# Kernel optimization log

Hardware: AMD Instinct MI355X
Metric: run time of the kernel (lower is better)

The kernel has to match this reference:

```python
import jax, jax.numpy as jnp
import numpy as np

N = 50000      # nodes
E = 400000     # edges
D_IN = 128     # input node feature dim
H = 128        # hidden_dim == node_dim inside layers
E_DIM = 16     # edge_attr dim
L = 3          # num_layers


def setup_inputs() -> dict:
    key = jax.random.key(0)
    ks = jax.random.split(key, 8)
    s = 0.05
    return {
        "x": jax.random.normal(ks[0], (N, D_IN), jnp.float32),
        "edge_attr": jax.random.normal(ks[1], (E, E_DIM), jnp.float32),
        "edge_index": jax.random.randint(ks[2], (2, E), 0, N),
        # learned params (W stored [in, out], i.e. transpose of torch Linear.weight)
        "proj_W": jax.random.normal(ks[3], (D_IN, H), jnp.float32) * s,
        "proj_b": jnp.zeros((H,), jnp.float32),
        "msg_W1": jax.random.normal(ks[4], (L, 2 * H + E_DIM, H), jnp.float32) * s,
        "msg_b1": jnp.zeros((L, H), jnp.float32),
        "msg_W2": jax.random.normal(ks[5], (L, H, H), jnp.float32) * s,
        "msg_b2": jnp.zeros((L, H), jnp.float32),
        "upd_W": jax.random.normal(ks[6], (L, 2 * H, H), jnp.float32) * s,
        "upd_b": jnp.zeros((L, H), jnp.float32),
        "ln_g": jnp.ones((L, H), jnp.float32),
        "ln_b": jnp.zeros((L, H), jnp.float32),
        "out_g": jnp.ones((H,), jnp.float32),
        "out_b": jnp.zeros((H,), jnp.float32),
    }


def _layernorm(x, g, b, eps=1e-5):
    mu = jnp.mean(x, axis=-1, keepdims=True)
    var = jnp.mean((x - mu) ** 2, axis=-1, keepdims=True)
    return (x - mu) * jax.lax.rsqrt(var + eps) * g + b


def reference(x, edge_attr, edge_index, proj_W, proj_b, msg_W1, msg_b1,
              msg_W2, msg_b2, upd_W, upd_b, ln_g, ln_b, out_g, out_b):
    i_idx, j_idx = edge_index[0], edge_index[1]
    h = x @ proj_W + proj_b                       # [N, H]
    for l in range(L):                            # fixed small layer count
        # gather + message MLP: m_ij = relu(relu([h_i, h_j, e_ij] W1) W2)
        m_in = jnp.concatenate([h[i_idx], h[j_idx], edge_attr], axis=-1)  # [E, 2H+E_DIM]
        m = jax.nn.relu(m_in @ msg_W1[l] + msg_b1[l])
        m = jax.nn.relu(m @ msg_W2[l] + msg_b2[l])  # [E, H]
        # scatter-add aggregate to destination nodes (index_add_ on i_idx)
        agg = jax.ops.segment_sum(m, i_idx, num_segments=N)  # [N, H]
        # node update MLP + residual + LayerNorm (dropout p inactive in eval)
        out = jax.nn.relu(jnp.concatenate([h, agg], axis=-1) @ upd_W[l] + upd_b[l])
        h = _layernorm(out + h, ln_g[l], ln_b[l])
    h = _layernorm(h, out_g, out_b)
    return jnp.mean(h, axis=0)[None, :]           # global mean pool -> [1, H]
```

## Files before the change

kernel.cpp:

```cpp
#include <hip/hip_runtime.h>
#include <math.h>

#define N_NODES 50000
#define N_EDGES 400000
#define DIM_IN  128
#define H       128
#define E_DIM   16
#define NLAYERS 3

#define K1      272
#define K1P     288
#define HS      136
#define GS      136
#define ES      40
#define US      264
#define PS      136
#define FPS     132
#define MB      32
#define UMB     64
#define NT_E    (N_EDGES / MB)
#define NSB     ((N_NODES + 255) / 256)

typedef short  s16x8 __attribute__((ext_vector_type(8)));
typedef float  f32x4 __attribute__((ext_vector_type(4)));

__device__ inline unsigned short f2bf(float f) {
    union { float f; unsigned u; } v; v.f = f;
    unsigned r = v.u + 0x7FFFu + ((v.u >> 16) & 1u);
    return (unsigned short)(r >> 16);
}
__device__ inline float bf2f(unsigned short u) {
    union { unsigned u; float f; } v; v.u = (unsigned)u << 16; return v.f;
}
__device__ inline uint4 addbf8(uint4 a, uint4 b) {
    union U { uint4 v; unsigned short s[8]; } ua, ub, uo;
    ua.v = a; ub.v = b;
#pragma unroll
    for (int i = 0; i < 8; ++i) uo.s[i] = f2bf(bf2f(ua.s[i]) + bf2f(ub.s[i]));
    return uo.v;
}

__global__ __launch_bounds__(256)
void convert_w1(const float* __restrict__ W1, unsigned short* __restrict__ W1t)
{
    const int o = blockIdx.x * 256 + threadIdx.x;
    const int l = o / (128 * K1P);
    const int r = o % (128 * K1P);
    const int n = r / K1P;
    const int k = r % K1P;
    const float v = (k < K1) ? W1[(size_t)l * K1 * H + (size_t)k * H + n] : 0.f;
    W1t[o] = f2bf(v);
}

__global__ __launch_bounds__(256)
void convert_w2(const float* __restrict__ W2, unsigned short* __restrict__ W2t)
{
    const int o = blockIdx.x * 256 + threadIdx.x;
    const int l = o / (H * H);
    const int r = o % (H * H);
    const int n = r / H;
    const int k = r % H;
    W2t[o] = f2bf(W2[(size_t)l * H * H + (size_t)k * H + n]);
}

__global__ __launch_bounds__(256)
void convert_wu(const float* __restrict__ Wu, unsigned short* __restrict__ Wut)
{
    const int o = blockIdx.x * 256 + threadIdx.x;
    const int l = o / (H * 256);
    const int r = o % (H * 256);
    const int n = r / 256;
    const int k = r % 256;
    Wut[o] = f2bf(Wu[(size_t)l * 256 * H + (size_t)k * H + n]);
}

__global__ __launch_bounds__(256)
void convert_wp(const float* __restrict__ Wp, unsigned short* __restrict__ Wpt)
{
    const int o = blockIdx.x * 256 + threadIdx.x;
    const int n = o / H;
    const int k = o % H;
    Wpt[o] = f2bf(Wp[(size_t)k * H + n]);
}

__global__ __launch_bounds__(256)
void convert_ea(const float* __restrict__ ea, const int* __restrict__ perm,
                unsigned short* __restrict__ eabf)
{
    const int o = blockIdx.x * 256 + threadIdx.x;
    const int p = o >> 3;
    const int j = (o & 7) * 2;
    const int pe = perm[p];
    const float2 v = *(const float2*)&ea[(size_t)pe * E_DIM + j];
    eabf[(size_t)p * E_DIM + j]     = f2bf(v.x);
    eabf[(size_t)p * E_DIM + j + 1] = f2bf(v.y);
}

__global__ __launch_bounds__(256)
void hist_kernel(const int* __restrict__ ei, int* __restrict__ hist)
{
    const int e = blockIdx.x * 256 + threadIdx.x;
    if (e < N_EDGES) atomicAdd(&hist[ei[e]], 1);
}

__global__ __launch_bounds__(256)
void blocksum_kernel(const int* __restrict__ hist, int* __restrict__ bsum)
{
    __shared__ int red[4];
    const int t = threadIdx.x;
    const int idx = blockIdx.x * 256 + t;
    int v = (idx < N_NODES) ? hist[idx] : 0;
#pragma unroll
    for (int off = 32; off > 0; off >>= 1) v += __shfl_xor(v, off, 64);
    if ((t & 63) == 0) red[t >> 6] = v;
    __syncthreads();
    if (t == 0) bsum[blockIdx.x] = red[0] + red[1] + red[2] + red[3];
}

__global__ __launch_bounds__(256)
void scan_bsum_kernel(const int* __restrict__ bsum, int* __restrict__ boff)
{
    __shared__ int s[256];
    const int t = threadIdx.x;
    const int v = (t < NSB) ? bsum[t] : 0;
    s[t] = v; __syncthreads();
    for (int off = 1; off < 256; off <<= 1) {
        const int u = (t >= off) ? s[t - off] : 0;
        __syncthreads();
        s[t] += u;
        __syncthreads();
    }
    if (t < NSB) boff[t] = s[t] - v;
}

__global__ __launch_bounds__(256)
void scan_final_kernel(const int* __restrict__ hist, const int* __restrict__ boff,
                       int* __restrict__ cursor)
{
    __shared__ int s[256];
    const int t = threadIdx.x;
    const int idx = blockIdx.x * 256 + t;
    const int v = (idx < N_NODES) ? hist[idx] : 0;
    s[t] = v; __syncthreads();
    for (int off = 1; off < 256; off <<= 1) {
        const int u = (t >= off) ? s[t - off] : 0;
        __syncthreads();
        s[t] += u;
        __syncthreads();
    }
    if (idx < N_NODES) cursor[idx] = boff[blockIdx.x] + s[t] - v;
}

__global__ __launch_bounds__(256)
void scatter_kernel(const int* __restrict__ ei, int* __restrict__ cursor,
                    int* __restrict__ i_s, int* __restrict__ j_s, int* __restrict__ perm)
{
    const int e = blockIdx.x * 256 + threadIdx.x;
    if (e < N_EDGES) {
        const int d = ei[e];
        const int p = atomicAdd(&cursor[d], 1);
        i_s[p] = d;
        j_s[p] = ei[N_EDGES + e];
        perm[p] = e;
    }
}

__global__ __launch_bounds__(256)
void proj_mfma(const float* __restrict__ x, const unsigned short* __restrict__ Wpt,
               const float* __restrict__ b, unsigned short* __restrict__ hbf)
{
    __shared__ __align__(16) unsigned short A[MB][PS];
    const int tid = threadIdx.x;
    const int n0 = blockIdx.x * MB;
    const int wave = tid >> 6, lane = tid & 63, l15 = lane & 15, l4 = lane >> 4;
    const int colbase = wave * 32;

#pragma unroll
    for (int i = 0; i < 4; ++i) {
        const int f = tid + i * 256;
        const int row = f >> 5, c4 = f & 31;
        const int node = min(n0 + row, N_NODES - 1);
        const float4 v = *((const float4*)(x + (size_t)node * DIM_IN) + c4);
        unsigned short o[4] = { f2bf(v.x), f2bf(v.y), f2bf(v.z), f2bf(v.w) };
        *(uint2*)&A[row][c4 * 4] = *(const uint2*)o;
    }
    __syncthreads();

    f32x4 acc[2][2];
#pragma unroll
    for (int mt = 0; mt < 2; ++mt)
#pragma unroll
        for (int nt = 0; nt < 2; ++nt) acc[mt][nt] = (f32x4)0.f;

    for (int k = 0; k < DIM_IN; k += 32) {
        const s16x8 a0 = *(const s16x8*)&A[l15][k + l4 * 8];
        const s16x8 a1 = *(const s16x8*)&A[16 + l15][k + l4 * 8];
        const s16x8 b0 = *(const s16x8*)&Wpt[(size_t)(colbase + l15) * DIM_IN + k + l4 * 8];
        const s16x8 b1 = *(const s16x8*)&Wpt[(size_t)(colbase + 16 + l15) * DIM_IN + k + l4 * 8];
        acc[0][0] = __builtin_amdgcn_mfma_f32_16x16x32_bf16(a0, b0, acc[0][0], 0, 0, 0);
        acc[0][1] = __builtin_amdgcn_mfma_f32_16x16x32_bf16(a0, b1, acc[0][1], 0, 0, 0);
        acc[1][0] = __builtin_amdgcn_mfma_f32_16x16x32_bf16(a1, b0, acc[1][0], 0, 0, 0);
        acc[1][1] = __builtin_amdgcn_mfma_f32_16x16x32_bf16(a1, b1, acc[1][1], 0, 0, 0);
    }

    const float bi0 = b[colbase + l15], bi1 = b[colbase + 16 + l15];
#pragma unroll
    for (int mt = 0; mt < 2; ++mt)
#pragma unroll
        for (int r = 0; r < 4; ++r) {
            const int row = mt * 16 + l4 * 4 + r;
            const int n = n0 + row;
            if (n < N_NODES) {
                hbf[(size_t)n * H + colbase + l15]      = f2bf(acc[mt][0][r] + bi0);
                hbf[(size_t)n * H + colbase + 16 + l15] = f2bf(acc[mt][1][r] + bi1);
            }
        }
}

__global__ __launch_bounds__(256)
void premul(const unsigned short* __restrict__ hbf,
            const unsigned short* __restrict__ W1t,
            unsigned short* __restrict__ Pa, unsigned short* __restrict__ Pb)
{
    __shared__ __align__(16) unsigned short A[MB][PS];
    const int tid = threadIdx.x;
    const int n0 = blockIdx.x * MB;
    const int wave = tid >> 6, lane = tid & 63, l15 = lane & 15, l4 = lane >> 4;
    const int colbase = wave * 32;

#pragma unroll
    for (int i = 0; i < 2; ++i) {
        const int f = tid + i * 256;
        const int row = f >> 4, c = f & 15;
        const int node = min(n0 + row, N_NODES - 1);
        const uint4 v = *((const uint4*)(hbf + (size_t)node * H) + c);
        *(uint4*)&A[row][c * 8] = v;
    }
    __syncthreads();

    f32x4 aa[2][2], ab[2][2];
#pragma unroll
    for (int mt = 0; mt < 2; ++mt)
#pragma unroll
        for (int nt = 0; nt < 2; ++nt) { aa[mt][nt] = (f32x4)0.f; ab[mt][nt] = (f32x4)0.f; }

#pragma unroll
    for (int kt = 0; kt < 4; ++kt) {
        const s16x8 a0 = *(const s16x8*)&A[l15][kt * 32 + l4 * 8];
        const s16x8 a1 = *(const s16x8*)&A[16 + l15][kt * 32 + l4 * 8];
        const s16x8 wa0 = *(const s16x8*)&W1t[(size_t)(colbase + l15) * K1P + kt * 32 + l4 * 8];
        const s16x8 wa1 = *(const s16x8*)&W1t[(size_t)(colbase + 16 + l15) * K1P + kt * 32 + l4 * 8];
        const s16x8 wb0 = *(const s16x8*)&W1t[(size_t)(colbase + l15) * K1P + 128 + kt * 32 + l4 * 8];
        const s16x8 wb1 = *(const s16x8*)&W1t[(size_t)(colbase + 16 + l15) * K1P + 128 + kt * 32 + l4 * 8];
        aa[0][0] = __builtin_amdgcn_mfma_f32_16x16x32_bf16(a0, wa0, aa[0][0], 0, 0, 0);
        aa[0][1] = __builtin_amdgcn_mfma_f32_16x16x32_bf16(a0, wa1, aa[0][1], 0, 0, 0);
        aa[1][0] = __builtin_amdgcn_mfma_f32_16x16x32_bf16(a1, wa0, aa[1][0], 0, 0, 0);
        aa[1][1] = __builtin_amdgcn_mfma_f32_16x16x32_bf16(a1, wa1, aa[1][1], 0, 0, 0);
        ab[0][0] = __builtin_amdgcn_mfma_f32_16x16x32_bf16(a0, wb0, ab[0][0], 0, 0, 0);
        ab[0][1] = __builtin_amdgcn_mfma_f32_16x16x32_bf16(a0, wb1, ab[0][1], 0, 0, 0);
        ab[1][0] = __builtin_amdgcn_mfma_f32_16x16x32_bf16(a1, wb0, ab[1][0], 0, 0, 0);
        ab[1][1] = __builtin_amdgcn_mfma_f32_16x16x32_bf16(a1, wb1, ab[1][1], 0, 0, 0);
    }

#pragma unroll
    for (int mt = 0; mt < 2; ++mt)
#pragma unroll
        for (int r = 0; r < 4; ++r) {
            const int row = mt * 16 + l4 * 4 + r;
            const int n = n0 + row;
            if (n < N_NODES) {
                Pa[(size_t)n * H + colbase + l15]      = f2bf(aa[mt][0][r]);
                Pa[(size_t)n * H + colbase + 16 + l15] = f2bf(aa[mt][1][r]);
                Pb[(size_t)n * H + colbase + l15]      = f2bf(ab[mt][0][r]);
                Pb[(size_t)n * H + colbase + 16 + l15] = f2bf(ab[mt][1][r]);
            }
        }
}

__global__ __launch_bounds__(256, 4)
void edge_kernel(const unsigned short* __restrict__ Pa,
                 const unsigned short* __restrict__ Pb,
                 const unsigned short* __restrict__ eabf,
                 const int*   __restrict__ i_s,
                 const int*   __restrict__ j_s,
                 const unsigned short* __restrict__ W1t,
                 const float* __restrict__ b1,
                 const unsigned short* __restrict__ W2t,
                 const float* __restrict__ b2,
                 float*       __restrict__ agg)
{
    __shared__ __align__(16) unsigned short Gsum[MB * GS];
    __shared__ __align__(16) unsigned short Et[MB * ES];
    __shared__ __align__(16) unsigned short Hid[MB * HS];
    __shared__ __align__(16) unsigned short Mbf[MB * HS];
    __shared__ int idxbuf[2][MB];

    const int tid  = threadIdx.x;
    const int wave = tid >> 6;
    const int lane = tid & 63;
    const int l15  = lane & 15;
    const int l4   = lane >> 4;
    const int colbase = wave * 32;

    const int sl_e = tid >> 4;
    const int sl_c = tid & 15;

    s16x8 w2f[2][4], w1cf[2];
#pragma unroll
    for (int kt = 0; kt < 4; ++kt) {
        w2f[0][kt] = *(const s16x8*)&W2t[(size_t)(colbase + l15) * H + kt * 32 + l4 * 8];
        w2f[1][kt] = *(const s16x8*)&W2t[(size_t)(colbase + 16 + l15) * H + kt * 32 + l4 * 8];
    }
    w1cf[0] = *(const s16x8*)&W1t[(size_t)(colbase + l15) * K1P + 256 + l4 * 8];
    w1cf[1] = *(const s16x8*)&W1t[(size_t)(colbase + 16 + l15) * K1P + 256 + l4 * 8];
    const float b1c0 = b1[colbase + l15], b1c1 = b1[colbase + 16 + l15];
    const float b2c0 = b2[colbase + l15], b2c1 = b2[colbase + 16 + l15];

    int t = blockIdx.x;
    if (t >= NT_E) return;

    {
#pragma unroll
        for (int i = 0; i < 2; ++i) {
            const int e = sl_e + i * 16;
            const int ni = i_s[t * MB + e];
            const int nj = j_s[t * MB + e];
            const uint4 va = *((const uint4*)(Pa + (size_t)ni * H) + sl_c);
            const uint4 vb = *((const uint4*)(Pb + (size_t)nj * H) + sl_c);
            *(uint4*)&Gsum[e * GS + sl_c * 8] = addbf8(va, vb);
        }
        if (tid < 64) {
            const uint4 ve = *((const uint4*)eabf + (size_t)t * 64 + tid);
            *(uint4*)&Et[(tid >> 1) * ES + (tid & 1) * 8] = ve;
        } else if (tid < 128) {
            const int tt = tid - 64;
            const uint4 z = {0, 0, 0, 0};
            *(uint4*)&Et[(tt >> 1) * ES + 16 + (tt & 1) * 8] = z;
        }
        if (tid < MB) idxbuf[0][tid] = i_s[t * MB + tid];
    }
    __syncthreads();

    int p = 0;
    for (; t < NT_E; t += gridDim.x, p ^= 1) {
        const int t1 = t + gridDim.x;

        uint4 pfa[2], pfb[2];
        uint4 pfe = {0, 0, 0, 0};
        int   pfi = 0;
        if (t1 < NT_E) {
#pragma unroll
            for (int i = 0; i < 2; ++i) {
                const int e = sl_e + i * 16;
                const int ni = i_s[t1 * MB + e];
                const int nj = j_s[t1 * MB + e];
                pfa[i] = *((const uint4*)(Pa + (size_t)ni * H) + sl_c);
                pfb[i] = *((const uint4*)(Pb + (size_t)nj * H) + sl_c);
            }
            if (tid < 64) pfe = *((const uint4*)eabf + (size_t)t1 * 64 + tid);
            if (tid < MB) pfi = i_s[t1 * MB + tid];
        }

        f32x4 acc[2][2];
#pragma unroll
        for (int mt = 0; mt < 2; ++mt)
#pragma unroll
            for (int nt = 0; nt < 2; ++nt) acc[mt][nt] = (f32x4)0.f;
        {
            const s16x8 a0 = *(const s16x8*)&Et[l15 * ES + l4 * 8];
            const s16x8 a1 = *(const s16x8*)&Et[(16 + l15) * ES + l4 * 8];
            acc[0][0] = __builtin_amdgcn_mfma_f32_16x16x32_bf16(a0, w1cf[0], acc[0][0], 0, 0, 0);
            acc[0][1] = __builtin_amdgcn_mfma_f32_16x16x32_bf16(a0, w1cf[1], acc[0][1], 0, 0, 0);
            acc[1][0] = __builtin_amdgcn_mfma_f32_16x16x32_bf16(a1, w1cf[0], acc[1][0], 0, 0, 0);
            acc[1][1] = __builtin_amdgcn_mfma_f32_16x16x32_bf16(a1, w1cf[1], acc[1][1], 0, 0, 0);
        }

#pragma unroll
        for (int mt = 0; mt < 2; ++mt)
#pragma unroll
            for (int r = 0; r < 4; ++r) {
                const int row = mt * 16 + l4 * 4 + r;
                const float g0 = bf2f(Gsum[row * GS + colbase + l15]);
                const float g1 = bf2f(Gsum[row * GS + colbase + 16 + l15]);
                Hid[row * HS + colbase + l15]      = f2bf(fmaxf(acc[mt][0][r] + g0 + b1c0, 0.f));
                Hid[row * HS + colbase + 16 + l15] = f2bf(fmaxf(acc[mt][1][r] + g1 + b1c1, 0.f));
            }
        __syncthreads();

        if (t1 < NT_E) {
#pragma unroll
            for (int i = 0; i < 2; ++i) {
                const int e = sl_e + i * 16;
                *(uint4*)&Gsum[e * GS + sl_c * 8] = addbf8(pfa[i], pfb[i]);
            }
            if (tid < 64)
                *(uint4*)&Et[(tid >> 1) * ES + (tid & 1) * 8] = pfe;
            if (tid < MB) idxbuf[p ^ 1][tid] = pfi;
        }

#pragma unroll
        for (int mt = 0; mt < 2; ++mt)
#pragma unroll
            for (int nt = 0; nt < 2; ++nt) acc[mt][nt] = (f32x4)0.f;

#pragma unroll
        for (int kt = 0; kt < 4; ++kt) {
            const s16x8 a0 = *(const s16x8*)&Hid[l15 * HS + kt * 32 + l4 * 8];
            const s16x8 a1 = *(const s16x8*)&Hid[(16 + l15) * HS + kt * 32 + l4 * 8];
            acc[0][0] = __builtin_amdgcn_mfma_f32_16x16x32_bf16(a0, w2f[0][kt], acc[0][0], 0, 0, 0);
            acc[0][1] = __builtin_amdgcn_mfma_f32_16x16x32_bf16(a0, w2f[1][kt], acc[0][1], 0, 0, 0);
            acc[1][0] = __builtin_amdgcn_mfma_f32_16x16x32_bf16(a1, w2f[0][kt], acc[1][0], 0, 0, 0);
            acc[1][1] = __builtin_amdgcn_mfma_f32_16x16x32_bf16(a1, w2f[1][kt], acc[1][1], 0, 0, 0);
        }

#pragma unroll
        for (int mt = 0; mt < 2; ++mt)
#pragma unroll
            for (int r = 0; r < 4; ++r) {
                const int row = mt * 16 + l4 * 4 + r;
                Mbf[row * HS + colbase + l15]      = f2bf(fmaxf(acc[mt][0][r] + b2c0, 0.f));
                Mbf[row * HS + colbase + 16 + l15] = f2bf(fmaxf(acc[mt][1][r] + b2c1, 0.f));
            }
        __syncthreads();

        {
            const int* idxp = idxbuf[p];
            const int c    = tid & 127;
            const int half = tid >> 7;
            int cur = idxp[half * 16];
            float s = 0.f;
            for (int r = half * 16; r < half * 16 + 16; ++r) {
                const int d = idxp[r];
                if (d != cur) {
                    atomicAdd(&agg[(size_t)cur * H + c], s);
                    s = 0.f; cur = d;
                }
                s += bf2f(Mbf[r * HS + c]);
            }
            atomicAdd(&agg[(size_t)cur * H + c], s);
        }
    }
}

__global__ __launch_bounds__(256, 3)
void update_mfma(unsigned short* __restrict__ hbf, float* __restrict__ agg,
                 const unsigned short* __restrict__ Wut, const float* __restrict__ b,
                 const float* __restrict__ g, const float* __restrict__ bln)
{
    __shared__ __align__(16) unsigned short A[UMB][US];
    float* Afp = (float*)&A[0][0];

    const int tid = threadIdx.x;
    const int n0 = blockIdx.x * UMB;
    const int wave = tid >> 6, lane = tid & 63, l15 = lane & 15, l4 = lane >> 4;
    const int colbase = wave * 32;

    s16x8 bf0[8], bf1[8];
#pragma unroll
    for (int kt = 0; kt < 8; ++kt) {
        bf0[kt] = *(const s16x8*)&Wut[(size_t)(colbase + l15) * 256 + kt * 32 + l4 * 8];
        bf1[kt] = *(const s16x8*)&Wut[(size_t)(colbase + 16 + l15) * 256 + kt * 32 + l4 * 8];
    }

#pragma unroll
    for (int i = 0; i < 4; ++i) {
        const int f = tid + i * 256;
        const int row = f >> 4, c = f & 15;
        const int node = min(n0 + row, N_NODES - 1);
        const uint4 v = *((const uint4*)(hbf + (size_t)node * H) + c);
        *(uint4*)&A[row][c * 8] = v;
    }
#pragma unroll
    for (int i = 0; i < 8; ++i) {
        const int f = tid + i * 256;
        const int row = f >> 5, c4 = f & 31;
        const int node = min(n0 + row, N_NODES - 1);
        float4* ap = (float4*)(agg + (size_t)node * H) + c4;
        const float4 v = *ap;
        if (n0 + row < N_NODES) {
            const float4 z = {0.f, 0.f, 0.f, 0.f};
            *ap = z;
        }
        unsigned short o[4] = { f2bf(v.x), f2bf(v.y), f2bf(v.z), f2bf(v.w) };
        *(uint2*)&A[row][128 + c4 * 4] = *(const uint2*)o;
    }
    __syncthreads();

    f32x4 acc[4][2];
#pragma unroll
    for (int mt = 0; mt < 4; ++mt) { acc[mt][0] = (f32x4)0.f; acc[mt][1] = (f32x4)0.f; }

#pragma unroll
    for (int kt = 0; kt < 8; ++kt) {
#pragma unroll
        for (int mt = 0; mt < 4; ++mt) {
            const s16x8 a = *(const s16x8*)&A[mt * 16 + l15][kt * 32 + l4 * 8];
            acc[mt][0] = __builtin_amdgcn_mfma_f32_16x16x32_bf16(a, bf0[kt], acc[mt][0], 0, 0, 0);
            acc[mt][1] = __builtin_amdgcn_mfma_f32_16x16x32_bf16(a, bf1[kt], acc[mt][1], 0, 0, 0);
        }
    }
    __syncthreads();

    {
        const float bi0 = b[colbase + l15], bi1 = b[colbase + 16 + l15];
#pragma unroll
        for (int mt = 0; mt < 4; ++mt)
#pragma unroll
            for (int r = 0; r < 4; ++r) {
                const int row = mt * 16 + l4 * 4 + r;
                Afp[row * FPS + colbase + l15]      = fmaxf(acc[mt][0][r] + bi0, 0.f);
                Afp[row * FPS + colbase + 16 + l15] = fmaxf(acc[mt][1][r] + bi1, 0.f);
            }
    }
    __syncthreads();

    const float g0 = g[lane],   g1 = g[64 + lane];
    const float l0 = bln[lane], l1 = bln[64 + lane];
    for (int q = 0; q < 16; ++q) {
        const int row = wave * 16 + q;
        const int n = n0 + row;
        if (n >= N_NODES) break;
        const float hr0 = bf2f(hbf[(size_t)n * H + lane]);
        const float hr1 = bf2f(hbf[(size_t)n * H + 64 + lane]);
        float v0 = Afp[row * FPS + lane]      + hr0;
        float v1 = Afp[row * FPS + 64 + lane] + hr1;
        float s = v0 + v1;
#pragma unroll
        for (int off = 32; off > 0; off >>= 1) s += __shfl_xor(s, off, 64);
        const float mu = s * (1.f / 128.f);
        const float d0 = v0 - mu, d1 = v1 - mu;
        float vs = d0 * d0 + d1 * d1;
#pragma unroll
        for (int off = 32; off > 0; off >>= 1) vs += __shfl_xor(vs, off, 64);
        const float inv = rsqrtf(vs * (1.f / 128.f) + 1e-5f);
        hbf[(size_t)n * H + lane]      = f2bf(d0 * inv * g0 + l0);
        hbf[(size_t)n * H + 64 + lane] = f2bf(d1 * inv * g1 + l1);
    }
}

__global__ __launch_bounds__(256)
void final_kernel(const unsigned short* __restrict__ hbf,
                  const float* __restrict__ g, const float* __restrict__ b,
                  float* __restrict__ out)
{
    __shared__ float red[4][128];
    const int tid = threadIdx.x;
    const int wave = tid >> 6, lane = tid & 63;
    const float g0 = g[lane], g1 = g[64 + lane];
    const float b0 = b[lane], b1 = b[64 + lane];
    float a0 = 0.f, a1 = 0.f;

    for (int n = blockIdx.x * 4 + wave; n < N_NODES; n += gridDim.x * 4) {
        const float v0 = bf2f(hbf[(size_t)n * H + lane]);
        const float v1 = bf2f(hbf[(size_t)n * H + 64 + lane]);
        float s = v0 + v1;
#pragma unroll
        for (int off = 32; off > 0; off >>= 1) s += __shfl_xor(s, off, 64);
        const float mu = s * (1.f / 128.f);
        const float d0 = v0 - mu, d1 = v1 - mu;
        float vs = d0 * d0 + d1 * d1;
#pragma unroll
        for (int off = 32; off > 0; off >>= 1) vs += __shfl_xor(vs, off, 64);
        const float inv = rsqrtf(vs * (1.f / 128.f) + 1e-5f);
        a0 += d0 * inv * g0 + b0;
        a1 += d1 * inv * g1 + b1;
    }
    red[wave][lane]      = a0;
    red[wave][64 + lane] = a1;
    __syncthreads();
    if (wave == 0) {
        const float s0 = red[0][lane] + red[1][lane] + red[2][lane] + red[3][lane];
        const float s1 = red[0][64 + lane] + red[1][64 + lane] + red[2][64 + lane] + red[3][64 + lane];
        atomicAdd(&out[lane],      s0 * (1.f / N_NODES));
        atomicAdd(&out[64 + lane], s1 * (1.f / N_NODES));
    }
}

extern "C" void kernel_launch(void* const* d_in, const int* in_sizes, int n_in,
                              void* d_out, int out_size, void* d_ws, size_t ws_size,
                              hipStream_t stream)
{
    const float* x         = (const float*)d_in[0];
    const float* edge_attr = (const float*)d_in[1];
    const int*   edge_idx  = (const int*)  d_in[2];
    const float* proj_W    = (const float*)d_in[3];
    const float* proj_b    = (const float*)d_in[4];
    const float* msg_W1    = (const float*)d_in[5];
    const float* msg_b1    = (const float*)d_in[6];
    const float* msg_W2    = (const float*)d_in[7];
    const float* msg_b2    = (const float*)d_in[8];
    const float* upd_W     = (const float*)d_in[9];
    const float* upd_b     = (const float*)d_in[10];
    const float* ln_g      = (const float*)d_in[11];
    const float* ln_b      = (const float*)d_in[12];
    const float* out_g     = (const float*)d_in[13];
    const float* out_b     = (const float*)d_in[14];
    float* out = (float*)d_out;

    char* w = (char*)d_ws;
    float* agg = (float*)w;                   w += (size_t)N_NODES * H * 4;
    unsigned short* hbf  = (unsigned short*)w; w += (size_t)N_NODES * H * 2;
    unsigned short* Pa   = (unsigned short*)w; w += (size_t)N_NODES * H * 2;
    unsigned short* Pb   = (unsigned short*)w; w += (size_t)N_NODES * H * 2;
    unsigned short* eabf = (unsigned short*)w; w += (size_t)N_EDGES * E_DIM * 2;
    unsigned short* W1t  = (unsigned short*)w; w += (size_t)NLAYERS * H * K1P * 2;
    unsigned short* W2t  = (unsigned short*)w; w += (size_t)NLAYERS * H * H * 2;
    unsigned short* Wut  = (unsigned short*)w; w += (size_t)NLAYERS * H * 256 * 2;
    unsigned short* Wpt  = (unsigned short*)w; w += (size_t)H * DIM_IN * 2;
    int* hist   = (int*)w;                    w += (size_t)N_NODES * 4;
    int* cursor = (int*)w;                    w += (size_t)N_NODES * 4;
    int* bsum   = (int*)w;                    w += (size_t)256 * 4;
    int* boff   = (int*)w;                    w += (size_t)256 * 4;
    int* i_s    = (int*)w;                    w += (size_t)N_EDGES * 4;
    int* j_s    = (int*)w;                    w += (size_t)N_EDGES * 4;
    int* perm   = (int*)w;                    w += (size_t)N_EDGES * 4;

    convert_w1<<<(NLAYERS * H * K1P) / 256, 256, 0, stream>>>(msg_W1, W1t);
    convert_w2<<<(NLAYERS * H * H) / 256, 256, 0, stream>>>(msg_W2, W2t);
    convert_wu<<<(NLAYERS * H * 256) / 256, 256, 0, stream>>>(upd_W, Wut);
    convert_wp<<<(H * DIM_IN) / 256, 256, 0, stream>>>(proj_W, Wpt);

    hipMemsetAsync(hist, 0, (size_t)N_NODES * 4, stream);
    hipMemsetAsync(agg, 0, (size_t)N_NODES * H * sizeof(float), stream);
    hist_kernel<<<(N_EDGES + 255) / 256, 256, 0, stream>>>(edge_idx, hist);
    blocksum_kernel<<<NSB, 256, 0, stream>>>(hist, bsum);
    scan_bsum_kernel<<<1, 256, 0, stream>>>(bsum, boff);
    scan_final_kernel<<<NSB, 256, 0, stream>>>(hist, boff, cursor);
    scatter_kernel<<<(N_EDGES + 255) / 256, 256, 0, stream>>>(edge_idx, cursor, i_s, j_s, perm);
    convert_ea<<<(N_EDGES * 8) / 256, 256, 0, stream>>>(edge_attr, perm, eabf);

    const int nblk = (N_NODES + MB - 1) / MB;
    proj_mfma<<<nblk, 256, 0, stream>>>(x, Wpt, proj_b, hbf);

    const int ublk = (N_NODES + UMB - 1) / UMB;
    for (int l = 0; l < NLAYERS; ++l) {
        premul<<<nblk, 256, 0, stream>>>(hbf, W1t + (size_t)l * H * K1P, Pa, Pb);
        edge_kernel<<<1024, 256, 0, stream>>>(
            Pa, Pb, eabf, i_s, j_s,
            W1t + (size_t)l * H * K1P, msg_b1 + (size_t)l * H,
            W2t + (size_t)l * H * H,   msg_b2 + (size_t)l * H, agg);
        update_mfma<<<ublk, 256, 0, stream>>>(
            hbf, agg, Wut + (size_t)l * H * 256, upd_b + (size_t)l * H,
            ln_g + (size_t)l * H, ln_b + (size_t)l * H);
    }

    hipMemsetAsync(out, 0, H * sizeof(float), stream);
    final_kernel<<<256, 256, 0, stream>>>(hbf, out_g, out_b, out);
}
```

Baseline: 535.7 us.

## Switch edge-kernel intermediates to fp16 and scatter directly from MFMA accumulators

```diff
diff --git a/kernel.cpp b/kernel.cpp
--- a/kernel.cpp
+++ b/kernel.cpp
@@ -11,8 +11,8 @@
 #define K1      272
 #define K1P     288
 #define HS      136
-#define GS      136
-#define ES      40
+#define GSH     136
+#define ETS     32
 #define US      264
 #define PS      136
 #define FPS     132
@@ -21,8 +21,10 @@
 #define NT_E    (N_EDGES / MB)
 #define NSB     ((N_NODES + 255) / 256)
 
-typedef short  s16x8 __attribute__((ext_vector_type(8)));
-typedef float  f32x4 __attribute__((ext_vector_type(4)));
+typedef short    s16x8 __attribute__((ext_vector_type(8)));
+typedef float    f32x4 __attribute__((ext_vector_type(4)));
+typedef _Float16 f16x8 __attribute__((ext_vector_type(8)));
+typedef __fp16   fp16x2 __attribute__((ext_vector_type(2)));
 
 __device__ inline unsigned short f2bf(float f) {
     union { float f; unsigned u; } v; v.f = f;
@@ -32,12 +34,18 @@
 __device__ inline float bf2f(unsigned short u) {
     union { unsigned u; float f; } v; v.u = (unsigned)u << 16; return v.f;
 }
-__device__ inline uint4 addbf8(uint4 a, uint4 b) {
-    union U { uint4 v; unsigned short s[8]; } ua, ub, uo;
-    ua.v = a; ub.v = b;
-#pragma unroll
-    for (int i = 0; i < 8; ++i) uo.s[i] = f2bf(bf2f(ua.s[i]) + bf2f(ub.s[i]));
-    return uo.v;
+__device__ inline unsigned pk2(float a, float b) {
+    union { fp16x2 h; unsigned u; } v;
+    v.h = __builtin_amdgcn_cvt_pkrtz(a, b);
+    return v.u;
+}
+__device__ inline float f16lo(unsigned u) {
+    union { unsigned short s; _Float16 h; } v; v.s = (unsigned short)(u & 0xffffu);
+    return (float)v.h;
+}
+__device__ inline float f16hi(unsigned u) {
+    union { unsigned short s; _Float16 h; } v; v.s = (unsigned short)(u >> 16);
+    return (float)v.h;
 }
 
 __global__ __launch_bounds__(256)
@@ -60,7 +68,10 @@
     const int r = o % (H * H);
     const int n = r / H;
     const int k = r % H;
-    W2t[o] = f2bf(W2[(size_t)l * H * H + (size_t)k * H + n]);
+    const int kp = (k & ~31) | ((k & 15) << 1) | ((k >> 4) & 1);
+    union { _Float16 h; unsigned short s; } v;
+    v.h = (_Float16)W2[(size_t)l * H * H + (size_t)k * H + n];
+    W2t[(size_t)l * H * H + (size_t)n * H + kp] = v.s;
 }
 
 __global__ __launch_bounds__(256)
@@ -269,15 +280,13 @@
             const int row = mt * 16 + l4 * 4 + r;
             const int n = n0 + row;
             if (n < N_NODES) {
-                Pa[(size_t)n * H + colbase + l15]      = f2bf(aa[mt][0][r]);
-                Pa[(size_t)n * H + colbase + 16 + l15] = f2bf(aa[mt][1][r]);
-                Pb[(size_t)n * H + colbase + l15]      = f2bf(ab[mt][0][r]);
-                Pb[(size_t)n * H + colbase + 16 + l15] = f2bf(ab[mt][1][r]);
+                *(unsigned*)&Pa[(size_t)n * H + colbase + 2 * l15] = pk2(aa[mt][0][r], aa[mt][1][r]);
+                *(unsigned*)&Pb[(size_t)n * H + colbase + 2 * l15] = pk2(ab[mt][0][r], ab[mt][1][r]);
             }
         }
 }
 
-__global__ __launch_bounds__(256, 4)
+__global__ __launch_bounds__(256, 5)
 void edge_kernel(const unsigned short* __restrict__ Pa,
                  const unsigned short* __restrict__ Pb,
                  const unsigned short* __restrict__ eabf,
@@ -289,10 +298,9 @@
                  const float* __restrict__ b2,
                  float*       __restrict__ agg)
 {
-    __shared__ __align__(16) unsigned short Gsum[MB * GS];
-    __shared__ __align__(16) unsigned short Et[MB * ES];
+    __shared__ __align__(16) unsigned short Gs[MB * GSH];
+    __shared__ __align__(16) unsigned short Et[MB * ETS];
     __shared__ __align__(16) unsigned short Hid[MB * HS];
-    __shared__ __align__(16) unsigned short Mbf[MB * HS];
     __shared__ int idxbuf[2][MB];
 
     const int tid  = threadIdx.x;
@@ -305,11 +313,12 @@
     const int sl_e = tid >> 4;
     const int sl_c = tid & 15;
 
-    s16x8 w2f[2][4], w1cf[2];
+    f16x8 w2f[2][4];
+    s16x8 w1cf[2];
 #pragma unroll
     for (int kt = 0; kt < 4; ++kt) {
-        w2f[0][kt] = *(const s16x8*)&W2t[(size_t)(colbase + l15) * H + kt * 32 + l4 * 8];
-        w2f[1][kt] = *(const s16x8*)&W2t[(size_t)(colbase + 16 + l15) * H + kt * 32 + l4 * 8];
+        w2f[0][kt] = *(const f16x8*)&W2t[(size_t)(colbase + l15) * H + kt * 32 + l4 * 8];
+        w2f[1][kt] = *(const f16x8*)&W2t[(size_t)(colbase + 16 + l15) * H + kt * 32 + l4 * 8];
     }
     w1cf[0] = *(const s16x8*)&W1t[(size_t)(colbase + l15) * K1P + 256 + l4 * 8];
     w1cf[1] = *(const s16x8*)&W1t[(size_t)(colbase + 16 + l15) * K1P + 256 + l4 * 8];
@@ -322,20 +331,22 @@
     {
 #pragma unroll
         for (int i = 0; i < 2; ++i) {
-            const int e = sl_e + i * 16;
+            const int e  = sl_e + i * 16;
             const int ni = i_s[t * MB + e];
             const int nj = j_s[t * MB + e];
-            const uint4 va = *((const uint4*)(Pa + (size_t)ni * H) + sl_c);
-            const uint4 vb = *((const uint4*)(Pb + (size_t)nj * H) + sl_c);
-            *(uint4*)&Gsum[e * GS + sl_c * 8] = addbf8(va, vb);
+            union { uint4 u; f16x8 h; } a, b, s;
+            a.u = *((const uint4*)(Pa + (size_t)ni * H) + sl_c);
+            b.u = *((const uint4*)(Pb + (size_t)nj * H) + sl_c);
+            s.h = a.h + b.h;
+            *(uint4*)&Gs[e * GSH + sl_c * 8] = s.u;
         }
         if (tid < 64) {
             const uint4 ve = *((const uint4*)eabf + (size_t)t * 64 + tid);
-            *(uint4*)&Et[(tid >> 1) * ES + (tid & 1) * 8] = ve;
+            *(uint4*)&Et[(tid >> 1) * ETS + (tid & 1) * 8] = ve;
         } else if (tid < 128) {
             const int tt = tid - 64;
             const uint4 z = {0, 0, 0, 0};
-            *(uint4*)&Et[(tt >> 1) * ES + 16 + (tt & 1) * 8] = z;
+            *(uint4*)&Et[(tt >> 1) * ETS + 16 + (tt & 1) * 8] = z;
         }
         if (tid < MB) idxbuf[0][tid] = i_s[t * MB + tid];
     }
@@ -352,10 +363,8 @@
 #pragma unroll
             for (int i = 0; i < 2; ++i) {
                 const int e = sl_e + i * 16;
-                const int ni = i_s[t1 * MB + e];
-                const int nj = j_s[t1 * MB + e];
-                pfa[i] = *((const uint4*)(Pa + (size_t)ni * H) + sl_c);
-                pfb[i] = *((const uint4*)(Pb + (size_t)nj * H) + sl_c);
+                pfa[i] = *((const uint4*)(Pa + (size_t)i_s[t1 * MB + e] * H) + sl_c);
+                pfb[i] = *((const uint4*)(Pb + (size_t)j_s[t1 * MB + e] * H) + sl_c);
             }
             if (tid < 64) pfe = *((const uint4*)eabf + (size_t)t1 * 64 + tid);
             if (tid < MB) pfi = i_s[t1 * MB + tid];
@@ -363,12 +372,13 @@
 
         f32x4 acc[2][2];
 #pragma unroll
-        for (int mt = 0; mt < 2; ++mt)
-#pragma unroll
-            for (int nt = 0; nt < 2; ++nt) acc[mt][nt] = (f32x4)0.f;
+        for (int mt = 0; mt < 2; ++mt) {
+            acc[mt][0] = (f32x4)(b1c0);
+            acc[mt][1] = (f32x4)(b1c1);
+        }
         {
-            const s16x8 a0 = *(const s16x8*)&Et[l15 * ES + l4 * 8];
-            const s16x8 a1 = *(const s16x8*)&Et[(16 + l15) * ES + l4 * 8];
+            const s16x8 a0 = *(const s16x8*)&Et[l15 * ETS + l4 * 8];
+            const s16x8 a1 = *(const s16x8*)&Et[(16 + l15) * ETS + l4 * 8];
             acc[0][0] = __builtin_amdgcn_mfma_f32_16x16x32_bf16(a0, w1cf[0], acc[0][0], 0, 0, 0);
             acc[0][1] = __builtin_amdgcn_mfma_f32_16x16x32_bf16(a0, w1cf[1], acc[0][1], 0, 0, 0);
             acc[1][0] = __builtin_amdgcn_mfma_f32_16x16x32_bf16(a1, w1cf[0], acc[1][0], 0, 0, 0);
@@ -380,10 +390,10 @@
 #pragma unroll
             for (int r = 0; r < 4; ++r) {
                 const int row = mt * 16 + l4 * 4 + r;
-                const float g0 = bf2f(Gsum[row * GS + colbase + l15]);
-                const float g1 = bf2f(Gsum[row * GS + colbase + 16 + l15]);
-                Hid[row * HS + colbase + l15]      = f2bf(fmaxf(acc[mt][0][r] + g0 + b1c0, 0.f));
-                Hid[row * HS + colbase + 16 + l15] = f2bf(fmaxf(acc[mt][1][r] + g1 + b1c1, 0.f));
+                const unsigned gv = *(const unsigned*)&Gs[row * GSH + colbase + 2 * l15];
+                const unsigned hh = pk2(fmaxf(acc[mt][0][r] + f16lo(gv), 0.f),
+                                        fmaxf(acc[mt][1][r] + f16hi(gv), 0.f));
+                *(unsigned*)&Hid[row * HS + colbase + 2 * l15] = hh;
             }
         __syncthreads();
 
@@ -391,53 +401,52 @@
 #pragma unroll
             for (int i = 0; i < 2; ++i) {
                 const int e = sl_e + i * 16;
-                *(uint4*)&Gsum[e * GS + sl_c * 8] = addbf8(pfa[i], pfb[i]);
+                union { uint4 u; f16x8 h; } a, b, s;
+                a.u = pfa[i]; b.u = pfb[i];
+                s.h = a.h + b.h;
+                *(uint4*)&Gs[e * GSH + sl_c * 8] = s.u;
             }
             if (tid < 64)
-                *(uint4*)&Et[(tid >> 1) * ES + (tid & 1) * 8] = pfe;
+                *(uint4*)&Et[(tid >> 1) * ETS + (tid & 1) * 8] = pfe;
             if (tid < MB) idxbuf[p ^ 1][tid] = pfi;
         }
 
 #pragma unroll
-        for (int mt = 0; mt < 2; ++mt)
-#pragma unroll
-            for (int nt = 0; nt < 2; ++nt) acc[mt][nt] = (f32x4)0.f;
-
+        for (int mt = 0; mt < 2; ++mt) {
+            acc[mt][0] = (f32x4)(b2c0);
+            acc[mt][1] = (f32x4)(b2c1);
+        }
 #pragma unroll
         for (int kt = 0; kt < 4; ++kt) {
-            const s16x8 a0 = *(const s16x8*)&Hid[l15 * HS + kt * 32 + l4 * 8];
-            const s16x8 a1 = *(const s16x8*)&Hid[(16 + l15) * HS + kt * 32 + l4 * 8];
-            acc[0][0] = __builtin_amdgcn_mfma_f32_16x16x32_bf16(a0, w2f[0][kt], acc[0][0], 0, 0, 0);
-            acc[0][1] = __builtin_amdgcn_mfma_f32_16x16x32_bf16(a0, w2f[1][kt], acc[0][1], 0, 0, 0);
-            acc[1][0] = __builtin_amdgcn_mfma_f32_16x16x32_bf16(a1, w2f[0][kt], acc[1][0], 0, 0, 0);
-            acc[1][1] = __builtin_amdgcn_mfma_f32_16x16x32_bf16(a1, w2f[1][kt], acc[1][1], 0, 0, 0);
-        }
-
-#pragma unroll
-        for (int mt = 0; mt < 2; ++mt)
-#pragma unroll
-            for (int r = 0; r < 4; ++r) {
-                const int row = mt * 16 + l4 * 4 + r;
-                Mbf[row * HS + colbase + l15]      = f2bf(fmaxf(acc[mt][0][r] + b2c0, 0.f));
-                Mbf[row * HS + colbase + 16 + l15] = f2bf(fmaxf(acc[mt][1][r] + b2c1, 0.f));
-            }
+            const f16x8 a0 = *(const f16x8*)&Hid[l15 * HS + kt * 32 + l4 * 8];
+            const f16x8 a1 = *(const f16x8*)&Hid[(16 + l15) * HS + kt * 32 + l4 * 8];
+            acc[0][0] = __builtin_amdgcn_mfma_f32_16x16x32_f16(a0, w2f[0][kt], acc[0][0], 0, 0, 0);
+            acc[0][1] = __builtin_amdgcn_mfma_f32_16x16x32_f16(a0, w2f[1][kt], acc[0][1], 0, 0, 0);
+            acc[1][0] = __builtin_amdgcn_mfma_f32_16x16x32_f16(a1, w2f[0][kt], acc[1][0], 0, 0, 0);
+            acc[1][1] = __builtin_amdgcn_mfma_f32_16x16x32_f16(a1, w2f[1][kt], acc[1][1], 0, 0, 0);
+        }
         __syncthreads();
 
         {
             const int* idxp = idxbuf[p];
-            const int c    = tid & 127;
-            const int half = tid >> 7;
-            int cur = idxp[half * 16];
-            float s = 0.f;
-            for (int r = half * 16; r < half * 16 + 16; ++r) {
-                const int d = idxp[r];
-                if (d != cur) {
-                    atomicAdd(&agg[(size_t)cur * H + c], s);
-                    s = 0.f; cur = d;
+#pragma unroll
+            for (int mt = 0; mt < 2; ++mt) {
+                const int rb = mt * 16 + l4 * 4;
+                const int d0 = idxp[rb],     d1 = idxp[rb + 1];
+                const int d2 = idxp[rb + 2], d3 = idxp[rb + 3];
+#pragma unroll
+                for (int nt = 0; nt < 2; ++nt) {
+                    const int col = colbase + nt * 16 + l15;
+                    float s = fmaxf(acc[mt][nt][0], 0.f);
+                    if (d1 != d0) { atomicAdd(&agg[(size_t)d0 * H + col], s); s = 0.f; }
+                    s += fmaxf(acc[mt][nt][1], 0.f);
+                    if (d2 != d1) { atomicAdd(&agg[(size_t)d1 * H + col], s); s = 0.f; }
+                    s += fmaxf(acc[mt][nt][2], 0.f);
+                    if (d3 != d2) { atomicAdd(&agg[(size_t)d2 * H + col], s); s = 0.f; }
+                    s += fmaxf(acc[mt][nt][3], 0.f);
+                    atomicAdd(&agg[(size_t)d3 * H + col], s);
                 }
-                s += bf2f(Mbf[r * HS + c]);
             }
-            atomicAdd(&agg[(size_t)cur * H + c], s);
         }
     }
 }
@@ -635,7 +644,7 @@
     const int ublk = (N_NODES + UMB - 1) / UMB;
     for (int l = 0; l < NLAYERS; ++l) {
         premul<<<nblk, 256, 0, stream>>>(hbf, W1t + (size_t)l * H * K1P, Pa, Pb);
-        edge_kernel<<<1024, 256, 0, stream>>>(
+        edge_kernel<<<1280, 256, 0, stream>>>(
             Pa, Pb, eabf, i_s, j_s,
             W1t + (size_t)l * H * K1P, msg_b1 + (size_t)l * H,
             W2t + (size_t)l * H * H,   msg_b2 + (size_t)l * H, agg);
```

Result: slower. 794.5 us (+48.3%).
